# Kernel optimization log

Measured on AMD Instinct MI355X. Metric: run time of the kernel, lower is better.

## Reference

```python
import jax, jax.numpy as jnp
import numpy as np

IN_SIZE = 1024
HID = 1024


def setup_inputs() -> dict:
    key = jax.random.key(0)
    ks = jax.random.split(key, 5)
    B, T = 32, 512
    bound = 1.0 / np.sqrt(HID)
    x = jax.random.normal(ks[0], (B, T, IN_SIZE), dtype=jnp.float32)
    h0 = jnp.zeros((B, HID), dtype=jnp.float32)
    c0 = jnp.zeros((B, HID), dtype=jnp.float32)
    W_ih = jax.random.uniform(ks[1], (4 * HID, IN_SIZE), minval=-bound, maxval=bound, dtype=jnp.float32)
    W_hh = jax.random.uniform(ks[2], (4 * HID, HID), minval=-bound, maxval=bound, dtype=jnp.float32)
    b_ih = jax.random.uniform(ks[3], (4 * HID,), minval=-bound, maxval=bound, dtype=jnp.float32)
    b_hh = jax.random.uniform(ks[4], (4 * HID,), minval=-bound, maxval=bound, dtype=jnp.float32)
    return {"x": x, "h0": h0, "c0": c0, "W_ih": W_ih, "W_hh": W_hh, "b_ih": b_ih, "b_hh": b_hh}


def _lstm_final_h(x, h0, c0, W_ih, W_hh, b_ih, b_hh):
    # Precompute input projections for all timesteps: [B,T,4H]
    xg = jnp.einsum('bti,gi->btg', x, W_ih) + b_ih + b_hh
    H = h0.shape[-1]

    def step(carry, xg_t):
        h, c = carry
        gates = xg_t + h @ W_hh.T  # [B,4H]
        i, f, g, o = jnp.split(gates, 4, axis=-1)  # torch LSTMCell gate order
        i = jax.nn.sigmoid(i)
        f = jax.nn.sigmoid(f)
        g = jnp.tanh(g)
        o = jax.nn.sigmoid(o)
        c_new = f * c + i * g
        h_new = o * jnp.tanh(c_new)
        return (h_new, c_new), None

    (h_final, _), _ = jax.lax.scan(step, (h0, c0), jnp.swapaxes(xg, 0, 1))
    return h_final


def reference(x, h0, c0, W_ih, W_hh, b_ih, b_hh):
    return _lstm_final_h(x, h0, c0, W_ih, W_hh, b_ih, b_hh)
```

## Files before the change

kernel.cpp:

```cpp
#include <hip/hip_runtime.h>
#include <stdint.h>

typedef __attribute__((ext_vector_type(8))) short short8;
typedef __attribute__((ext_vector_type(4))) float f32x4;

__device__ __forceinline__ unsigned short f32_to_bf16(float f) {
    unsigned int u = __float_as_uint(f);
    unsigned int r = (u + 0x7FFF + ((u >> 16) & 1)) >> 16;
    return (unsigned short)r;
}
__device__ __forceinline__ float bf16_to_f32(unsigned short s) {
    return __uint_as_float(((unsigned int)s) << 16);
}

__device__ __forceinline__ float sigm_fast(float z) {
    return __fdividef(1.f, 1.f + __expf(-z));
}
__device__ __forceinline__ float tanh_fast(float z) {
    float a = fabsf(z);
    float e = __expf(-2.f * a);
    float r = __fdividef(1.f - e, 1.f + e);
    return copysignf(r, z);
}

__global__ void cvt_bf16_kernel(const float* __restrict__ in,
                                unsigned short* __restrict__ out, int n) {
    int i = (blockIdx.x * blockDim.x + threadIdx.x) * 4;
    if (i >= n) return;
    float4 v = *(const float4*)(in + i);
    ushort4 o;
    o.x = f32_to_bf16(v.x);
    o.y = f32_to_bf16(v.y);
    o.z = f32_to_bf16(v.z);
    o.w = f32_to_bf16(v.w);
    *(ushort4*)(out + i) = o;
}

__global__ void bias_add_kernel(const float* __restrict__ bi,
                                const float* __restrict__ bh,
                                float* __restrict__ bias) {
    int i = blockIdx.x * blockDim.x + threadIdx.x;
    bias[i] = bi[i] + bh[i];
}

__global__ void fill_kernel(unsigned int* __restrict__ p, unsigned int v, int n) {
    int i = blockIdx.x * blockDim.x + threadIdx.x;
    if (i < n) p[i] = v;
}

__global__ void hG_init_kernel(const float* __restrict__ h0,
                               unsigned int* __restrict__ hG) {
    int D = blockIdx.x * blockDim.x + threadIdx.x;
    int i2 = D & 3, b = (D >> 2) & 31, kq = D >> 7;
    int j = kq * 8 + i2 * 2;
    unsigned int lo = f32_to_bf16(h0[b * 1024 + j]);
    unsigned int hi = f32_to_bf16(h0[b * 1024 + j + 1]);
    hG[D] = lo | (hi << 16);
}

#define LDP 40

__global__ __launch_bounds__(256) void gemm_xproj(
    const unsigned short* __restrict__ A,
    const unsigned short* __restrict__ B,
    const float* __restrict__ bias,
    unsigned short* __restrict__ C) {
    __shared__ unsigned short As[64][LDP];
    __shared__ unsigned short Bs[64][LDP];
    const int tid  = threadIdx.x;
    const int lane = tid & 63;
    const int wave = tid >> 6;
    const int m0 = blockIdx.y * 64;
    const int n0 = blockIdx.x * 64;
    const int wm = (wave & 1) * 32;
    const int wn = (wave >> 1) * 32;

    f32x4 acc[2][2] = {};

    const int sr = tid >> 2;
    const int sk = (tid & 3) * 8;
    const int fr = lane & 15;
    const int fk = (lane >> 4) * 8;

    for (int k0 = 0; k0 < 1024; k0 += 32) {
        uint4 av = *(const uint4*)&A[(m0 + sr) * 1024 + k0 + sk];
        uint4 bv = *(const uint4*)&B[(n0 + sr) * 1024 + k0 + sk];
        __syncthreads();
        *(uint4*)&As[sr][sk] = av;
        *(uint4*)&Bs[sr][sk] = bv;
        __syncthreads();
        short8 a0 = *(const short8*)&As[wm + fr][fk];
        short8 a1 = *(const short8*)&As[wm + 16 + fr][fk];
        short8 b0 = *(const short8*)&Bs[wn + fr][fk];
        short8 b1 = *(const short8*)&Bs[wn + 16 + fr][fk];
        acc[0][0] = __builtin_amdgcn_mfma_f32_16x16x32_bf16(a0, b0, acc[0][0], 0, 0, 0);
        acc[0][1] = __builtin_amdgcn_mfma_f32_16x16x32_bf16(a0, b1, acc[0][1], 0, 0, 0);
        acc[1][0] = __builtin_amdgcn_mfma_f32_16x16x32_bf16(a1, b0, acc[1][0], 0, 0, 0);
        acc[1][1] = __builtin_amdgcn_mfma_f32_16x16x32_bf16(a1, b1, acc[1][1], 0, 0, 0);
    }

    const int col = lane & 15;
    const int rq  = (lane >> 4) * 4;
    for (int mt = 0; mt < 2; mt++) {
        for (int nt = 0; nt < 2; nt++) {
            int gcol = n0 + wn + nt * 16 + col;
            float bv = bias[gcol];
            for (int r = 0; r < 4; r++) {
                int grow = m0 + wm + mt * 16 + rq + r;
                C[(size_t)grow * 4096 + gcol] = f32_to_bf16(acc[mt][nt][r] + bv);
            }
        }
    }
}

__global__ __launch_bounds__(512, 1) void lstm_persist(
    const float* __restrict__ Whh,
    const unsigned short* __restrict__ xg,
    const float* __restrict__ c0,
    unsigned int* __restrict__ hSeq,
    float* __restrict__ out) {
    __shared__ float partial[2][4][4][32][20];

    const int tid  = threadIdx.x;
    const int bid  = blockIdx.x;
    const int j0   = bid * 16;
    const int lane = tid & 63;
    const int wave = tid >> 6;
    const int ks   = wave >> 1;
    const int nt   = wave & 1;
    const int col  = lane & 15;
    const int quad = lane >> 4;

    short8 af[4][8];
#pragma unroll
    for (int mt = 0; mt < 4; ++mt) {
#pragma unroll
        for (int u = 0; u < 8; ++u) {
            const float* wr = Whh + (size_t)(mt * 1024 + j0 + col) * 1024
                              + (ks * 8 + u) * 32 + quad * 8;
            float4 wa = *(const float4*)wr;
            float4 wb = *(const float4*)(wr + 4);
            short8 v;
            v[0] = (short)f32_to_bf16(wa.x); v[1] = (short)f32_to_bf16(wa.y);
            v[2] = (short)f32_to_bf16(wa.z); v[3] = (short)f32_to_bf16(wa.w);
            v[4] = (short)f32_to_bf16(wb.x); v[5] = (short)f32_to_bf16(wb.y);
            v[6] = (short)f32_to_bf16(wb.z); v[7] = (short)f32_to_bf16(wb.w);
            af[mt][u] = v;
        }
        asm volatile("" ::: "memory");
    }

    const int eb = tid >> 4;
    const int ej = tid & 15;
    float cst = c0[eb * 1024 + j0 + ej];

    const int kq0  = bid * 2;
    const int bofs = nt * 16 + col;
    const int poff = ((kq0 + (ej >> 3)) * 32 + eb) * 4 + ((ej & 7) >> 1);

    __syncthreads();

    for (int t = 0; t < 512; ++t) {
        const unsigned int* hR = hSeq + ((size_t)t << 14);

        const unsigned short* px = xg + (size_t)(eb * 512 + t) * 4096 + j0 + ej;
        unsigned short x0 = px[0];
        unsigned short x1 = px[1024];
        unsigned short x2 = px[2048];
        unsigned short x3 = px[3072];

        uint4 bv[8];
        for (;;) {
#pragma unroll
            for (int u = 0; u < 8; ++u) {
                int kc = ks * 8 + u;
                const unsigned int* p = hR + ((kc * 4 + quad) * 32 + bofs) * 4;
                asm volatile("global_load_dwordx4 %0, %1, off sc1"
                             : "=v"(bv[u]) : "v"(p) : "memory");
            }
            asm volatile("s_waitcnt vmcnt(0)" ::: "memory");
            __builtin_amdgcn_sched_barrier(0);
            bool ok = true;
#pragma unroll
            for (int u = 0; u < 8; ++u)
                ok = ok && (bv[u].x != 0xFFFFFFFFu) && (bv[u].y != 0xFFFFFFFFu) &&
                           (bv[u].z != 0xFFFFFFFFu) && (bv[u].w != 0xFFFFFFFFu);
            if (__all(ok)) break;
            __builtin_amdgcn_s_sleep(1);
        }

        f32x4 acc[4] = {};
#pragma unroll
        for (int u = 0; u < 8; ++u) {
            union { uint4 u4; short8 s8; } cv;
            cv.u4 = bv[u];
#pragma unroll
            for (int mt = 0; mt < 4; ++mt)
                acc[mt] = __builtin_amdgcn_mfma_f32_16x16x32_bf16(af[mt][u], cv.s8,
                                                                  acc[mt], 0, 0, 0);
        }
        const int p = t & 1;
#pragma unroll
        for (int mt = 0; mt < 4; ++mt)
            *(f32x4*)&partial[p][ks][mt][bofs][quad * 4] = acc[mt];
        __syncthreads();

        float z[4];
#pragma unroll
        for (int q = 0; q < 4; ++q)
            z[q] = partial[p][0][q][eb][ej] + partial[p][1][q][eb][ej] +
                   partial[p][2][q][eb][ej] + partial[p][3][q][eb][ej];
        z[0] += bf16_to_f32(x0);
        z[1] += bf16_to_f32(x1);
        z[2] += bf16_to_f32(x2);
        z[3] += bf16_to_f32(x3);
        float ig = sigm_fast(z[0]);
        float fg = sigm_fast(z[1]);
        float gg = tanh_fast(z[2]);
        float og = sigm_fast(z[3]);
        cst = fg * cst + ig * gg;
        float hn = og * tanh_fast(cst);
        if (t == 511) {
            out[eb * 1024 + j0 + ej] = hn;
            break;
        }

        float hp = __shfl_xor(hn, 1);
        unsigned lo16 = f32_to_bf16(hn), hi16 = f32_to_bf16(hp);
        unsigned pack = lo16 | (hi16 << 16);
        unsigned int* pw = hSeq + ((size_t)(t + 1) << 14) + poff;
        if ((ej & 1) == 0) {
            asm volatile("global_store_dword %0, %1, off sc1\n\ts_waitcnt vmcnt(0)"
                         :: "v"(pw), "v"(pack) : "memory");
        }
    }
}

extern "C" void kernel_launch(void* const* d_in, const int* in_sizes, int n_in,
                              void* d_out, int out_size, void* d_ws, size_t ws_size,
                              hipStream_t stream) {
    const float* x    = (const float*)d_in[0];
    const float* h0   = (const float*)d_in[1];
    const float* c0   = (const float*)d_in[2];
    const float* Wih  = (const float*)d_in[3];
    const float* Whh  = (const float*)d_in[4];
    const float* b_ih = (const float*)d_in[5];
    const float* b_hh = (const float*)d_in[6];
    float* out = (float*)d_out;
    char* ws = (char*)d_ws;

    unsigned short* xg   = (unsigned short*)(ws);
    unsigned short* xA   = (unsigned short*)(ws + 134217728);
    unsigned short* wB   = (unsigned short*)(ws + 167772160);
    float*          bias = (float*)(ws + 176160768);
    unsigned int*   hSeq = (unsigned int*)(ws + 134217728);

    cvt_bf16_kernel<<<16384, 256, 0, stream>>>(x, xA, 16777216);
    cvt_bf16_kernel<<<4096, 256, 0, stream>>>(Wih, wB, 4194304);
    bias_add_kernel<<<16, 256, 0, stream>>>(b_ih, b_hh, bias);

    dim3 g1(64, 256);
    gemm_xproj<<<g1, 256, 0, stream>>>(xA, wB, bias, xg);

    fill_kernel<<<32704, 256, 0, stream>>>(hSeq + 16384, 0xFFFFFFFFu, 511 * 16384);
    hG_init_kernel<<<64, 256, 0, stream>>>(h0, hSeq);

    lstm_persist<<<64, 512, 0, stream>>>(Whh, xg, c0, hSeq, out);
}
```

Before: 1.924 ms.

## Replace sentinel-polling on h with per-wave flag array and prefetch next xg

The persistent LSTM kernel no longer polls the whole h buffer for 0xFFFFFFFF sentinels. Each wave now writes a per-step ready flag, wave 0 polls the 512 flags for the next step and releases the other waves through a shared-memory counter, and then h is loaded once. This drops the large sentinel fill of hSeq and shrinks the polling traffic. The xg values for the next step are also prefetched one step ahead to take their latency off the critical path. In exchange it adds a flag store per wave plus an intra-block spin on LDS, and it relies on h stores becoming visible before the flag store.

```diff
diff --git a/kernel.cpp b/kernel.cpp
--- a/kernel.cpp
+++ b/kernel.cpp
@@ -118,8 +118,10 @@
     const unsigned short* __restrict__ xg,
     const float* __restrict__ c0,
     unsigned int* __restrict__ hSeq,
+    unsigned int* __restrict__ flags,
     float* __restrict__ out) {
     __shared__ float partial[2][4][4][32][20];
+    __shared__ unsigned ready;
 
     const int tid  = threadIdx.x;
     const int bid  = blockIdx.x;
@@ -130,6 +132,8 @@
     const int nt   = wave & 1;
     const int col  = lane & 15;
     const int quad = lane >> 4;
+
+    if (tid == 0) ready = 0u;
 
     short8 af[4][8];
 #pragma unroll
@@ -154,39 +158,55 @@
     const int ej = tid & 15;
     float cst = c0[eb * 1024 + j0 + ej];
 
-    const int kq0  = bid * 2;
     const int bofs = nt * 16 + col;
-    const int poff = ((kq0 + (ej >> 3)) * 32 + eb) * 4 + ((ej & 7) >> 1);
+    const int poff = ((bid * 2 + (ej >> 3)) * 32 + eb) * 4 + ((ej & 7) >> 1);
 
     __syncthreads();
 
+    const unsigned short* px0 = xg + (size_t)(eb * 512) * 4096 + j0 + ej;
+    unsigned short xc0 = px0[0];
+    unsigned short xc1 = px0[1024];
+    unsigned short xc2 = px0[2048];
+    unsigned short xc3 = px0[3072];
+
     for (int t = 0; t < 512; ++t) {
+        if (wave == 0) {
+            const unsigned int* fp = flags + t * 512 + lane * 8;
+            uint4 fa, fb;
+            for (;;) {
+                asm volatile("global_load_dwordx4 %0, %2, off sc1\n\t"
+                             "global_load_dwordx4 %1, %2, off offset:16 sc1"
+                             : "=&v"(fa), "=&v"(fb) : "v"(fp) : "memory");
+                asm volatile("s_waitcnt vmcnt(0)" ::: "memory");
+                __builtin_amdgcn_sched_barrier(0);
+                unsigned andv = fa.x & fa.y & fa.z & fa.w & fb.x & fb.y & fb.z & fb.w;
+                if (__all(andv != 0u)) break;
+                __builtin_amdgcn_s_sleep(1);
+            }
+            if (lane == 0) *(volatile unsigned*)&ready = (unsigned)(t + 1);
+        } else {
+            while (*(volatile unsigned*)&ready < (unsigned)(t + 1)) {}
+        }
+
         const unsigned int* hR = hSeq + ((size_t)t << 14);
-
-        const unsigned short* px = xg + (size_t)(eb * 512 + t) * 4096 + j0 + ej;
-        unsigned short x0 = px[0];
-        unsigned short x1 = px[1024];
-        unsigned short x2 = px[2048];
-        unsigned short x3 = px[3072];
-
         uint4 bv[8];
-        for (;;) {
-#pragma unroll
-            for (int u = 0; u < 8; ++u) {
-                int kc = ks * 8 + u;
-                const unsigned int* p = hR + ((kc * 4 + quad) * 32 + bofs) * 4;
-                asm volatile("global_load_dwordx4 %0, %1, off sc1"
-                             : "=v"(bv[u]) : "v"(p) : "memory");
-            }
-            asm volatile("s_waitcnt vmcnt(0)" ::: "memory");
-            __builtin_amdgcn_sched_barrier(0);
-            bool ok = true;
-#pragma unroll
-            for (int u = 0; u < 8; ++u)
-                ok = ok && (bv[u].x != 0xFFFFFFFFu) && (bv[u].y != 0xFFFFFFFFu) &&
-                           (bv[u].z != 0xFFFFFFFFu) && (bv[u].w != 0xFFFFFFFFu);
-            if (__all(ok)) break;
-            __builtin_amdgcn_s_sleep(1);
+#pragma unroll
+        for (int u = 0; u < 8; ++u) {
+            int kc = ks * 8 + u;
+            const unsigned int* p = hR + ((kc * 4 + quad) * 32 + bofs) * 4;
+            asm volatile("global_load_dwordx4 %0, %1, off sc1"
+                         : "=v"(bv[u]) : "v"(p) : "memory");
+        }
+        asm volatile("s_waitcnt vmcnt(0)" ::: "memory");
+        __builtin_amdgcn_sched_barrier(0);
+
+        unsigned short nx0 = 0, nx1 = 0, nx2 = 0, nx3 = 0;
+        if (t < 511) {
+            const unsigned short* px = xg + (size_t)(eb * 512 + t + 1) * 4096 + j0 + ej;
+            nx0 = px[0];
+            nx1 = px[1024];
+            nx2 = px[2048];
+            nx3 = px[3072];
         }
 
         f32x4 acc[4] = {};
@@ -210,10 +230,10 @@
         for (int q = 0; q < 4; ++q)
             z[q] = partial[p][0][q][eb][ej] + partial[p][1][q][eb][ej] +
                    partial[p][2][q][eb][ej] + partial[p][3][q][eb][ej];
-        z[0] += bf16_to_f32(x0);
-        z[1] += bf16_to_f32(x1);
-        z[2] += bf16_to_f32(x2);
-        z[3] += bf16_to_f32(x3);
+        z[0] += bf16_to_f32(xc0);
+        z[1] += bf16_to_f32(xc1);
+        z[2] += bf16_to_f32(xc2);
+        z[3] += bf16_to_f32(xc3);
         float ig = sigm_fast(z[0]);
         float fg = sigm_fast(z[1]);
         float gg = tanh_fast(z[2]);
@@ -233,6 +253,13 @@
             asm volatile("global_store_dword %0, %1, off sc1\n\ts_waitcnt vmcnt(0)"
                          :: "v"(pw), "v"(pack) : "memory");
         }
+        if (lane == 0) {
+            unsigned one = 1u;
+            unsigned int* fw = flags + (t + 1) * 512 + bid * 8 + wave;
+            asm volatile("global_store_dword %0, %1, off sc1\n\ts_waitcnt vmcnt(0)"
+                         :: "v"(fw), "v"(one) : "memory");
+        }
+        xc0 = nx0; xc1 = nx1; xc2 = nx2; xc3 = nx3;
     }
 }
 
@@ -249,11 +276,12 @@
     float* out = (float*)d_out;
     char* ws = (char*)d_ws;
 
-    unsigned short* xg   = (unsigned short*)(ws);
-    unsigned short* xA   = (unsigned short*)(ws + 134217728);
-    unsigned short* wB   = (unsigned short*)(ws + 167772160);
-    float*          bias = (float*)(ws + 176160768);
-    unsigned int*   hSeq = (unsigned int*)(ws + 134217728);
+    unsigned short* xg    = (unsigned short*)(ws);
+    unsigned short* xA    = (unsigned short*)(ws + 134217728);
+    unsigned short* wB    = (unsigned short*)(ws + 167772160);
+    float*          bias  = (float*)(ws + 176160768);
+    unsigned int*   hSeq  = (unsigned int*)(ws + 134217728);
+    unsigned int*   flags = (unsigned int*)(ws + 167772160);
 
     cvt_bf16_kernel<<<16384, 256, 0, stream>>>(x, xA, 16777216);
     cvt_bf16_kernel<<<4096, 256, 0, stream>>>(Wih, wB, 4194304);
@@ -262,8 +290,9 @@
     dim3 g1(64, 256);
     gemm_xproj<<<g1, 256, 0, stream>>>(xA, wB, bias, xg);
 
-    fill_kernel<<<32704, 256, 0, stream>>>(hSeq + 16384, 0xFFFFFFFFu, 511 * 16384);
+    fill_kernel<<<2, 256, 0, stream>>>(flags, 1u, 512);
+    fill_kernel<<<1022, 256, 0, stream>>>(flags + 512, 0u, 511 * 512);
     hG_init_kernel<<<64, 256, 0, stream>>>(h0, hSeq);
 
-    lstm_persist<<<64, 512, 0, stream>>>(Whh, xg, c0, hSeq, out);
-}
+    lstm_persist<<<64, 512, 0, stream>>>(Whh, xg, c0, hSeq, flags, out);
+}
```

Measured after the change: 2.367 ms. 23.0% more time.

## Enlarge x-projection GEMM tiles to 128x128 and load tiles directly into LDS

Applied to the files above, without the earlier changes.

The input-projection GEMM moves from 64x64 to 128x128 block tiles. Each wave now computes a 64x64 sub-tile with 16 MFMA accumulators, which raises data reuse per LDS load. Global-to-LDS copies use global_load_lds, so staging data no longer passes through registers. The LDS rows lose their padding, which can cause bank conflicts, and loads are still not double-buffered.

```diff
diff --git a/kernel.cpp b/kernel.cpp
--- a/kernel.cpp
+++ b/kernel.cpp
@@ -58,54 +58,68 @@
     hG[D] = lo | (hi << 16);
 }
 
-#define LDP 40
-
 __global__ __launch_bounds__(256) void gemm_xproj(
     const unsigned short* __restrict__ A,
     const unsigned short* __restrict__ B,
     const float* __restrict__ bias,
     unsigned short* __restrict__ C) {
-    __shared__ unsigned short As[64][LDP];
-    __shared__ unsigned short Bs[64][LDP];
+    __shared__ unsigned short As[128][32];
+    __shared__ unsigned short Bs[128][32];
     const int tid  = threadIdx.x;
     const int lane = tid & 63;
     const int wave = tid >> 6;
-    const int m0 = blockIdx.y * 64;
-    const int n0 = blockIdx.x * 64;
-    const int wm = (wave & 1) * 32;
-    const int wn = (wave >> 1) * 32;
-
-    f32x4 acc[2][2] = {};
-
-    const int sr = tid >> 2;
-    const int sk = (tid & 3) * 8;
+    const int m0 = blockIdx.y * 128;
+    const int n0 = blockIdx.x * 128;
+    const int wm = (wave & 1) * 64;
+    const int wn = (wave >> 1) * 64;
+
+    f32x4 acc[4][4] = {};
+
+    const int srow = wave * 16 + (lane >> 2);
+    const int scol = (lane & 3) * 8;
+    const unsigned short* gA0 = A + (size_t)(m0 + srow) * 1024 + scol;
+    const unsigned short* gA1 = A + (size_t)(m0 + srow + 64) * 1024 + scol;
+    const unsigned short* gB0 = B + (size_t)(n0 + srow) * 1024 + scol;
+    const unsigned short* gB1 = B + (size_t)(n0 + srow + 64) * 1024 + scol;
+    unsigned short* lA0 = &As[wave * 16][0];
+    unsigned short* lA1 = &As[64 + wave * 16][0];
+    unsigned short* lB0 = &Bs[wave * 16][0];
+    unsigned short* lB1 = &Bs[64 + wave * 16][0];
+
     const int fr = lane & 15;
-    const int fk = (lane >> 4) * 8;
+    const int fo = (lane >> 4) * 8;
 
     for (int k0 = 0; k0 < 1024; k0 += 32) {
-        uint4 av = *(const uint4*)&A[(m0 + sr) * 1024 + k0 + sk];
-        uint4 bv = *(const uint4*)&B[(n0 + sr) * 1024 + k0 + sk];
         __syncthreads();
-        *(uint4*)&As[sr][sk] = av;
-        *(uint4*)&Bs[sr][sk] = bv;
+        __builtin_amdgcn_global_load_lds(gA0 + k0, lA0, 16, 0, 0);
+        __builtin_amdgcn_global_load_lds(gA1 + k0, lA1, 16, 0, 0);
+        __builtin_amdgcn_global_load_lds(gB0 + k0, lB0, 16, 0, 0);
+        __builtin_amdgcn_global_load_lds(gB1 + k0, lB1, 16, 0, 0);
+        asm volatile("s_waitcnt vmcnt(0)" ::: "memory");
         __syncthreads();
-        short8 a0 = *(const short8*)&As[wm + fr][fk];
-        short8 a1 = *(const short8*)&As[wm + 16 + fr][fk];
-        short8 b0 = *(const short8*)&Bs[wn + fr][fk];
-        short8 b1 = *(const short8*)&Bs[wn + 16 + fr][fk];
-        acc[0][0] = __builtin_amdgcn_mfma_f32_16x16x32_bf16(a0, b0, acc[0][0], 0, 0, 0);
-        acc[0][1] = __builtin_amdgcn_mfma_f32_16x16x32_bf16(a0, b1, acc[0][1], 0, 0, 0);
-        acc[1][0] = __builtin_amdgcn_mfma_f32_16x16x32_bf16(a1, b0, acc[1][0], 0, 0, 0);
-        acc[1][1] = __builtin_amdgcn_mfma_f32_16x16x32_bf16(a1, b1, acc[1][1], 0, 0, 0);
+
+        short8 a[4], b[4];
+#pragma unroll
+        for (int mt = 0; mt < 4; ++mt)
+            a[mt] = *(const short8*)&As[wm + mt * 16 + fr][fo];
+#pragma unroll
+        for (int nt = 0; nt < 4; ++nt)
+            b[nt] = *(const short8*)&Bs[wn + nt * 16 + fr][fo];
+#pragma unroll
+        for (int mt = 0; mt < 4; ++mt)
+#pragma unroll
+            for (int nt = 0; nt < 4; ++nt)
+                acc[mt][nt] = __builtin_amdgcn_mfma_f32_16x16x32_bf16(
+                    a[mt], b[nt], acc[mt][nt], 0, 0, 0);
     }
 
     const int col = lane & 15;
     const int rq  = (lane >> 4) * 4;
-    for (int mt = 0; mt < 2; mt++) {
-        for (int nt = 0; nt < 2; nt++) {
-            int gcol = n0 + wn + nt * 16 + col;
-            float bv = bias[gcol];
-            for (int r = 0; r < 4; r++) {
+    for (int nt = 0; nt < 4; ++nt) {
+        int gcol = n0 + wn + nt * 16 + col;
+        float bv = bias[gcol];
+        for (int mt = 0; mt < 4; ++mt) {
+            for (int r = 0; r < 4; ++r) {
                 int grow = m0 + wm + mt * 16 + rq + r;
                 C[(size_t)grow * 4096 + gcol] = f32_to_bf16(acc[mt][nt][r] + bv);
             }
@@ -154,9 +168,8 @@
     const int ej = tid & 15;
     float cst = c0[eb * 1024 + j0 + ej];
 
-    const int kq0  = bid * 2;
     const int bofs = nt * 16 + col;
-    const int poff = ((kq0 + (ej >> 3)) * 32 + eb) * 4 + ((ej & 7) >> 1);
+    const int poff = ((bid * 2 + (ej >> 3)) * 32 + eb) * 4 + ((ej & 7) >> 1);
 
     __syncthreads();
 
@@ -259,7 +272,7 @@
     cvt_bf16_kernel<<<4096, 256, 0, stream>>>(Wih, wB, 4194304);
     bias_add_kernel<<<16, 256, 0, stream>>>(b_ih, b_hh, bias);
 
-    dim3 g1(64, 256);
+    dim3 g1(32, 128);
     gemm_xproj<<<g1, 256, 0, stream>>>(xA, wB, bias, xg);
 
     fill_kernel<<<32704, 256, 0, stream>>>(hSeq + 16384, 0xFFFFFFFFu, 511 * 16384);
```

Result: faster. 1.810 ms (-6.0%).
